# Kernel tuning notes

Measured on AMD Instinct MI355X. Metric: run time of the kernel, lower is better.

## Reference

```python
import jax, jax.numpy as jnp
import numpy as np

B, T, E, H, S = 4, 4096, 1024, 16, 64
D = E // H  # head_dim = 64


def setup_inputs() -> dict:
    key = jax.random.key(0)
    ks = jax.random.split(key, 8)
    sc = 0.02
    return {
        "x": jax.random.normal(ks[0], (B, T, E), jnp.float32),
        "state": jax.random.normal(ks[1], (H, B, S), jnp.float32),
        # stacked per-head params (torch Linear weight layout [out, in])
        "A_w": jax.random.normal(ks[2], (H, S, S), jnp.float32) * sc,
        "A_b": jnp.zeros((H, S), jnp.float32),
        "C_w": jax.random.normal(ks[3], (H, D, S), jnp.float32) * sc,
        "C_b": jnp.zeros((H, D), jnp.float32),
        "sm": jax.random.uniform(ks[4], (H, S, D), jnp.float32),  # torch.rand init
        "Wo": jax.random.normal(ks[5], (E, E), jnp.float32) * sc,
        "bo": jnp.zeros((E,), jnp.float32),
    }


def reference(x, state, A_w, A_b, C_w, C_b, sm, Wo, bo):
    b, t, e = x.shape
    h, s = A_b.shape
    d = e // h
    xh = x.reshape(b, t, h, d)  # [B,T,H,D]
    # A(state): state[i].detach() @ A_w[i].T + A_b[i]  -> [H,B,S]
    a_state = jnp.einsum('hbj,hij->hbi', jax.lax.stop_gradient(state), A_w) + A_b[:, None, :]
    # semiseparable_matrix @ x_head^T, transposed back: [B,T,H,S]
    proj = jnp.einsum('hsd,bthd->bths', sm, xh)
    # broadcast A(state) over the sequence dim (faithful to the original)
    new_state = proj + a_state.transpose(1, 0, 2)[:, None]  # [B,T,H,S]
    # C(new_state): [B,T,H,D]
    out_h = jnp.einsum('bths,hds->bthd', new_state, C_w) + C_b
    # concat heads + output projection
    out = out_h.reshape(b, t, e) @ Wo.T + bo  # [B,T,E]
    new_state_stacked = new_state.transpose(2, 0, 1, 3)  # [H,B,T,S]
    return out, new_state_stacked
```

## Files before the change

kernel.cpp:

```cpp
#include <hip/hip_runtime.h>

#define Bz 4
#define Tz 4096
#define Ez 1024
#define Hz 16
#define Sz 64
#define Dz 64
#define MTz (Bz*Tz)

using f32x4  = __attribute__((ext_vector_type(4))) float;
using short8 = __attribute__((ext_vector_type(8))) short;

__device__ __forceinline__ unsigned f2bf(float f){
  unsigned u = __builtin_bit_cast(unsigned, f);
  u = u + 0x7FFFu + ((u >> 16) & 1u);
  return (u >> 16);
}

#define GLL16(gp, lp) __builtin_amdgcn_global_load_lds( \
    (const __attribute__((address_space(1))) unsigned int*)(gp), \
    (__attribute__((address_space(3))) unsigned int*)(lp), 16, 0, 0)

__global__ __launch_bounds__(256) void k1_pre(const float* __restrict__ state,
                                              const float* __restrict__ A_w,
                                              const float* __restrict__ A_b,
                                              const float* __restrict__ C_w,
                                              const float* __restrict__ sm,
                                              float* __restrict__ a_state,
                                              float* __restrict__ Mh,
                                              unsigned short* __restrict__ smB){
  const int blk = blockIdx.x, tid = threadIdx.x;
  const int h = blk >> 2, q4 = blk & 3;
  {
    const int d = q4*16 + (tid >> 4), dp0 = (tid & 15)*4;
    const float* cw  = C_w + (size_t)(h*64 + d)*64;
    const float* smh = sm + (size_t)h*4096 + dp0;
    float ax=0.f, ay=0.f, az=0.f, aw=0.f;
    #pragma unroll 8
    for (int s = 0; s < 64; ++s){
      float c = cw[s];
      float4 m4 = *(const float4*)&smh[s*64];
      ax += c*m4.x; ay += c*m4.y; az += c*m4.z; aw += c*m4.w;
    }
    *(float4*)&Mh[(size_t)h*4096 + d*64 + dp0] = make_float4(ax,ay,az,aw);
  }
  {
    int gi = blk*1024 + tid*4;
    float4 v = *(const float4*)&sm[gi];
    uint2 pk = make_uint2(f2bf(v.x) | (f2bf(v.y)<<16), f2bf(v.z) | (f2bf(v.w)<<16));
    *(uint2*)&smB[gi] = pk;
  }
  if (q4 == 0){
    const int b = tid >> 6, s = tid & 63;
    const float* aw = A_w + (size_t)(h*64 + s)*64;
    const float* st = state + (size_t)(h*4 + b)*64;
    float a0=A_b[h*64+s], a1=0.f, a2=0.f, a3=0.f;
    #pragma unroll 4
    for (int j = 0; j < 64; j += 4){
      a0 += aw[j]*st[j]; a1 += aw[j+1]*st[j+1];
      a2 += aw[j+2]*st[j+2]; a3 += aw[j+3]*st[j+3];
    }
    a_state[(h*4 + b)*64 + s] = (a0+a1)+(a2+a3);
  }
}

__global__ __launch_bounds__(256) void k2_pre(const float* __restrict__ Wo,
                                              const float* __restrict__ Mh,
                                              const float* __restrict__ C_w,
                                              const float* __restrict__ C_b,
                                              const float* __restrict__ a_state,
                                              unsigned short* __restrict__ Wb,
                                              float* __restrict__ bias_f){
  const int blk = blockIdx.x, tid = threadIdx.x;
  if (blk < 1024){
    const int e = blk, h = tid >> 4, dp0 = (tid & 15)*4;
    const float* wo = Wo + (size_t)e*1024 + h*64;
    const float* mh = Mh + (size_t)h*4096 + dp0;
    float ax=0.f, ay=0.f, az=0.f, aw=0.f;
    #pragma unroll 8
    for (int d = 0; d < 64; ++d){
      float c = wo[d];
      float4 m4 = *(const float4*)&mh[d*64];
      ax += c*m4.x; ay += c*m4.y; az += c*m4.z; aw += c*m4.w;
    }
    uint2 pk = make_uint2(f2bf(ax) | (f2bf(ay)<<16), f2bf(az) | (f2bf(aw)<<16));
    *(uint2*)&Wb[(size_t)e*1024 + h*64 + dp0] = pk;
  } else {
    int o = (blk - 1024)*256 + tid;
    int b = o >> 10, f = o & 1023;
    int h = f >> 6, d = f & 63;
    const float* cw = C_w + (size_t)(h*64 + d)*64;
    const float* as = a_state + (size_t)(h*4 + b)*64;
    float a0=C_b[h*64+d], a1=0.f, a2=0.f, a3=0.f;
    #pragma unroll 4
    for (int s = 0; s < 64; s += 4){
      a0 += cw[s]*as[s]; a1 += cw[s+1]*as[s+1];
      a2 += cw[s+2]*as[s+2]; a3 += cw[s+3]*as[s+3];
    }
    bias_f[o] = (a0+a1)+(a2+a3);
  }
}

__global__ __launch_bounds__(64) void k3_const(const float* __restrict__ Wo,
                                               const float* __restrict__ bo,
                                               const float* __restrict__ bias_f,
                                               float* __restrict__ constb){
  const int blk = blockIdx.x, tid = threadIdx.x;
  const int b = blk >> 4, e = (blk & 15)*64 + tid;
  const float4* wo = (const float4*)(Wo + (size_t)e*1024);
  const float4* bf = (const float4*)(bias_f + (size_t)b*1024);
  float ax=0.f, ay=0.f, az=0.f, aw=0.f;
  for (int f4 = 0; f4 < 256; ++f4){
    float4 w = wo[f4], v = bf[f4];
    ax += w.x*v.x; ay += w.y*v.y; az += w.z*v.z; aw += w.w*v.w;
  }
  constb[b*1024 + e] = bo[e] + ((ax+ay)+(az+aw));
}

__global__ __launch_bounds__(256) void k4_ns(const float* __restrict__ x,
                                             const unsigned short* __restrict__ smB,
                                             const float* __restrict__ a_state,
                                             unsigned short* __restrict__ xb,
                                             float* __restrict__ out2){
  __shared__ alignas(16) unsigned short Xs[128*72];
  __shared__ alignas(16) unsigned short Ss[64*72];
  const int lin = blockIdx.x;
  const int tb = lin & 31, h = (lin >> 5) & 15, b = lin >> 9;
  const int tid = threadIdx.x;
  const int lane = tid & 63, w = tid >> 6;
  const int l15 = lane & 15, l4 = lane >> 4;

  {
    const unsigned short* src = smB + (size_t)h*4096;
    #pragma unroll
    for (int cc = 0; cc < 2; ++cc){
      int c = tid*2 + cc;
      int s = c >> 3, seg = c & 7;
      *(uint4*)&Ss[s*72 + seg*8] = *(const uint4*)&src[s*64 + seg*8];
    }
  }
  {
    const int row0 = b*Tz + tb*128;
    #pragma unroll
    for (int it = 0; it < 4; ++it){
      int id = it*256 + tid;
      int r = id >> 3, c8 = id & 7;
      const float* px = x + (size_t)(row0 + r)*1024 + h*64 + c8*8;
      float4 v0 = *(const float4*)px, v1 = *(const float4*)(px + 4);
      uint4 pk;
      pk.x = f2bf(v0.x) | (f2bf(v0.y)<<16);
      pk.y = f2bf(v0.z) | (f2bf(v0.w)<<16);
      pk.z = f2bf(v1.x) | (f2bf(v1.y)<<16);
      pk.w = f2bf(v1.z) | (f2bf(v1.w)<<16);
      *(uint4*)&Xs[r*72 + c8*8] = pk;
      *(uint4*)(xb + (size_t)(row0 + r)*1024 + h*64 + c8*8) = pk;
    }
  }
  __syncthreads();

  f32x4 acc[2][4];
  #pragma unroll
  for (int j = 0; j < 4; ++j){
    float4 as4 = *(const float4*)&a_state[(h*4 + b)*64 + j*16 + l4*4];
    f32x4 a0; a0[0]=as4.x; a0[1]=as4.y; a0[2]=as4.z; a0[3]=as4.w;
    acc[0][j] = a0; acc[1][j] = a0;
  }
  #pragma unroll
  for (int kk = 0; kk < 2; ++kk){
    short8 a[2], bb[4];
    #pragma unroll
    for (int i = 0; i < 2; ++i)
      a[i] = *(const short8*)(&Xs[(w*32 + i*16 + l15)*72 + kk*32 + l4*8]);
    #pragma unroll
    for (int j = 0; j < 4; ++j)
      bb[j] = *(const short8*)(&Ss[(j*16 + l15)*72 + kk*32 + l4*8]);
    #pragma unroll
    for (int i = 0; i < 2; ++i)
      #pragma unroll
      for (int j = 0; j < 4; ++j)
        acc[i][j] = __builtin_amdgcn_mfma_f32_16x16x32_bf16(bb[j], a[i], acc[i][j], 0, 0, 0);
  }
  const size_t base = (size_t)h*1048576 + ((size_t)b*4096 + tb*128)*64;
  #pragma unroll
  for (int i = 0; i < 2; ++i)
    #pragma unroll
    for (int j = 0; j < 4; ++j){
      float4 o = make_float4(acc[i][j][0], acc[i][j][1], acc[i][j][2], acc[i][j][3]);
      *(float4*)(out2 + base + (size_t)(w*32 + i*16 + l15)*64 + j*16 + l4*4) = o;
    }
}

__global__ __launch_bounds__(512, 2) void k5_gemm(const unsigned short* __restrict__ xb,
                                                  const unsigned short* __restrict__ Wb,
                                                  const float* __restrict__ constb,
                                                  float* __restrict__ out){
  __shared__ alignas(16) unsigned short lds[4][2][8192];
  const int blk = blockIdx.x;
  const int swz = (blk & 7)*32 + (blk >> 3);
  const int bm = (swz >> 2)*256, bn = (swz & 3)*256;
  const int tid = threadIdx.x;
  const int lane = tid & 63, w = tid >> 6;
  const int l15 = lane & 15, l4 = lane >> 4;
  const int wr = w >> 2, wc = w & 3;

  const unsigned short* srcA[2];
  const unsigned short* srcB[2];
  #pragma unroll
  for (int q = 0; q < 2; ++q){
    int L = q*512 + w*64 + lane;
    int b = ((L>>2)&1) ^ ((L>>4)&1);
    int r = (L>>3)*2 + b;
    int g = (L&3) ^ ((((L>>3)&1)<<1) | b);
    srcA[q] = xb + (size_t)(bm + r)*1024 + g*8;
    srcB[q] = Wb + (size_t)(bn + r)*1024 + g*8;
  }
  const int dstoff = w*64*8;
  const int lane_off = ((l15*4 + l4) ^ (l15 & 7))*8;

  #pragma unroll
  for (int t = 0; t < 3; ++t){
    #pragma unroll
    for (int q = 0; q < 2; ++q) GLL16(srcA[q] + t*32, &lds[t][0][q*4096 + dstoff]);
    #pragma unroll
    for (int q = 0; q < 2; ++q) GLL16(srcB[q] + t*32, &lds[t][1][q*4096 + dstoff]);
  }
  asm volatile("s_waitcnt vmcnt(8)" ::: "memory");
  __builtin_amdgcn_s_barrier();
  asm volatile("" ::: "memory");

  f32x4 acc[8][4] = {};

  for (int t = 0; t < 32; ++t){
    const unsigned short* At = &lds[t & 3][0][0];
    const unsigned short* Bt = &lds[t & 3][1][0];
    const int ts = (t + 3) & 3;
    short8 bfr[4], afr[4];
    #pragma unroll
    for (int j = 0; j < 4; ++j)
      bfr[j] = *(const short8*)(Bt + (wc*64 + j*16)*32 + lane_off);
    #pragma unroll
    for (int i = 0; i < 4; ++i)
      afr[i] = *(const short8*)(At + (wr*128 + i*16)*32 + lane_off);
    if (t < 29){
      #pragma unroll
      for (int q = 0; q < 2; ++q) GLL16(srcA[q] + (t+3)*32, &lds[ts][0][q*4096 + dstoff]);
    }
    __builtin_amdgcn_s_setprio(1);
    #pragma unroll
    for (int i = 0; i < 4; ++i)
      #pragma unroll
      for (int j = 0; j < 4; ++j)
        acc[i][j] = __builtin_amdgcn_mfma_f32_16x16x32_bf16(bfr[j], afr[i], acc[i][j], 0, 0, 0);
    __builtin_amdgcn_s_setprio(0);
    #pragma unroll
    for (int i = 0; i < 4; ++i)
      afr[i] = *(const short8*)(At + (wr*128 + (4 + i)*16)*32 + lane_off);
    if (t < 29){
      #pragma unroll
      for (int q = 0; q < 2; ++q) GLL16(srcB[q] + (t+3)*32, &lds[ts][1][q*4096 + dstoff]);
    }
    __builtin_amdgcn_s_setprio(1);
    #pragma unroll
    for (int i = 0; i < 4; ++i)
      #pragma unroll
      for (int j = 0; j < 4; ++j)
        acc[4+i][j] = __builtin_amdgcn_mfma_f32_16x16x32_bf16(bfr[j], afr[i], acc[4+i][j], 0, 0, 0);
    __builtin_amdgcn_s_setprio(0);
    if (t < 29)       asm volatile("s_waitcnt vmcnt(8)" ::: "memory");
    else if (t == 29) asm volatile("s_waitcnt vmcnt(4)" ::: "memory");
    else if (t == 30) asm volatile("s_waitcnt vmcnt(0)" ::: "memory");
    if (t < 31){
      __builtin_amdgcn_s_barrier();
      asm volatile("" ::: "memory");
    }
  }

  const int bb = bm >> 12;
  #pragma unroll
  for (int j = 0; j < 4; ++j){
    int n0 = bn + wc*64 + j*16 + l4*4;
    float4 cv = *(const float4*)&constb[bb*1024 + n0];
    #pragma unroll
    for (int i = 0; i < 8; ++i){
      int trow = bm + wr*128 + i*16 + l15;
      float4 o = make_float4(acc[i][j][0] + cv.x, acc[i][j][1] + cv.y,
                             acc[i][j][2] + cv.z, acc[i][j][3] + cv.w);
      *(float4*)(out + (size_t)trow*1024 + n0) = o;
    }
  }
}

extern "C" void kernel_launch(void* const* d_in, const int* in_sizes, int n_in,
                              void* d_out, int out_size, void* d_ws, size_t ws_size,
                              hipStream_t stream){
  const float* x     = (const float*)d_in[0];
  const float* state = (const float*)d_in[1];
  const float* A_w   = (const float*)d_in[2];
  const float* A_b   = (const float*)d_in[3];
  const float* C_w   = (const float*)d_in[4];
  const float* C_b   = (const float*)d_in[5];
  const float* sm    = (const float*)d_in[6];
  const float* Wo    = (const float*)d_in[7];
  const float* bo    = (const float*)d_in[8];
  float* out  = (float*)d_out;
  float* out2 = out + (size_t)MTz*Ez;

  char* ws = (char*)d_ws;
  float* a_state          = (float*)(ws + 0);
  float* Mh               = (float*)(ws + 16384);
  float* bias_f           = (float*)(ws + 278528);
  float* constb           = (float*)(ws + 294912);
  unsigned short* smB     = (unsigned short*)(ws + 311296);
  unsigned short* Wb      = (unsigned short*)(ws + 442368);
  unsigned short* xb      = (unsigned short*)(ws + 2539520);

  k1_pre<<<64, 256, 0, stream>>>(state, A_w, A_b, C_w, sm, a_state, Mh, smB);
  k2_pre<<<1040, 256, 0, stream>>>(Wo, Mh, C_w, C_b, a_state, Wb, bias_f);
  k3_const<<<64, 64, 0, stream>>>(Wo, bo, bias_f, constb);
  k4_ns<<<2048, 256, 0, stream>>>(x, smB, a_state, xb, out2);
  k5_gemm<<<256, 512, 0, stream>>>(xb, Wb, constb, out);
}
```

Baseline: 119.1 us.

## Fragment-major A layout loaded directly to registers; merge precompute kernels

k4_ns now writes the bf16 activations in an MFMA-fragment-major layout. The GEMM reads its A operand straight from global memory into double-buffered registers, so only B is staged through LDS, which cuts LDS traffic and footprint. The five launches become four: the precompute kernels are merged into two, and the sm-to-bf16 conversion moves into k4_ns. The risk is exposed global-load latency on A, and the merged precompute kernels now run on far fewer blocks (16 and 80), which may serialize them.

```diff
diff --git a/kernel.cpp b/kernel.cpp
--- a/kernel.cpp
+++ b/kernel.cpp
@@ -21,18 +21,34 @@
     (const __attribute__((address_space(1))) unsigned int*)(gp), \
     (__attribute__((address_space(3))) unsigned int*)(lp), 16, 0, 0)
 
-__global__ __launch_bounds__(256) void k1_pre(const float* __restrict__ state,
+__global__ __launch_bounds__(256) void p0_pre(const float* __restrict__ state,
                                               const float* __restrict__ A_w,
                                               const float* __restrict__ A_b,
                                               const float* __restrict__ C_w,
+                                              const float* __restrict__ C_b,
                                               const float* __restrict__ sm,
                                               float* __restrict__ a_state,
                                               float* __restrict__ Mh,
-                                              unsigned short* __restrict__ smB){
-  const int blk = blockIdx.x, tid = threadIdx.x;
-  const int h = blk >> 2, q4 = blk & 3;
+                                              float* __restrict__ bias_f){
+  __shared__ float asl[4][64];
+  const int h = blockIdx.x, tid = threadIdx.x;
   {
-    const int d = q4*16 + (tid >> 4), dp0 = (tid & 15)*4;
+    const int b = tid >> 6, s = tid & 63;
+    const float* aw = A_w + (size_t)(h*64 + s)*64;
+    const float* st = state + (size_t)(h*4 + b)*64;
+    float a0=A_b[h*64+s], a1=0.f, a2=0.f, a3=0.f;
+    #pragma unroll 4
+    for (int j = 0; j < 64; j += 4){
+      a0 += aw[j]*st[j]; a1 += aw[j+1]*st[j+1];
+      a2 += aw[j+2]*st[j+2]; a3 += aw[j+3]*st[j+3];
+    }
+    float v = (a0+a1)+(a2+a3);
+    a_state[(h*4 + b)*64 + s] = v;
+    asl[b][s] = v;
+  }
+  #pragma unroll
+  for (int q = 0; q < 4; ++q){
+    const int d = q*16 + (tid >> 4), dp0 = (tid & 15)*4;
     const float* cw  = C_w + (size_t)(h*64 + d)*64;
     const float* smh = sm + (size_t)h*4096 + dp0;
     float ax=0.f, ay=0.f, az=0.f, aw=0.f;
@@ -44,83 +60,67 @@
     }
     *(float4*)&Mh[(size_t)h*4096 + d*64 + dp0] = make_float4(ax,ay,az,aw);
   }
+  __syncthreads();
   {
-    int gi = blk*1024 + tid*4;
-    float4 v = *(const float4*)&sm[gi];
-    uint2 pk = make_uint2(f2bf(v.x) | (f2bf(v.y)<<16), f2bf(v.z) | (f2bf(v.w)<<16));
-    *(uint2*)&smB[gi] = pk;
-  }
-  if (q4 == 0){
-    const int b = tid >> 6, s = tid & 63;
-    const float* aw = A_w + (size_t)(h*64 + s)*64;
-    const float* st = state + (size_t)(h*4 + b)*64;
-    float a0=A_b[h*64+s], a1=0.f, a2=0.f, a3=0.f;
-    #pragma unroll 4
-    for (int j = 0; j < 64; j += 4){
-      a0 += aw[j]*st[j]; a1 += aw[j+1]*st[j+1];
-      a2 += aw[j+2]*st[j+2]; a3 += aw[j+3]*st[j+3];
-    }
-    a_state[(h*4 + b)*64 + s] = (a0+a1)+(a2+a3);
-  }
-}
-
-__global__ __launch_bounds__(256) void k2_pre(const float* __restrict__ Wo,
-                                              const float* __restrict__ Mh,
-                                              const float* __restrict__ C_w,
-                                              const float* __restrict__ C_b,
-                                              const float* __restrict__ a_state,
-                                              unsigned short* __restrict__ Wb,
-                                              float* __restrict__ bias_f){
-  const int blk = blockIdx.x, tid = threadIdx.x;
-  if (blk < 1024){
-    const int e = blk, h = tid >> 4, dp0 = (tid & 15)*4;
-    const float* wo = Wo + (size_t)e*1024 + h*64;
-    const float* mh = Mh + (size_t)h*4096 + dp0;
-    float ax=0.f, ay=0.f, az=0.f, aw=0.f;
-    #pragma unroll 8
-    for (int d = 0; d < 64; ++d){
-      float c = wo[d];
-      float4 m4 = *(const float4*)&mh[d*64];
-      ax += c*m4.x; ay += c*m4.y; az += c*m4.z; aw += c*m4.w;
-    }
-    uint2 pk = make_uint2(f2bf(ax) | (f2bf(ay)<<16), f2bf(az) | (f2bf(aw)<<16));
-    *(uint2*)&Wb[(size_t)e*1024 + h*64 + dp0] = pk;
-  } else {
-    int o = (blk - 1024)*256 + tid;
-    int b = o >> 10, f = o & 1023;
-    int h = f >> 6, d = f & 63;
+    const int b = tid >> 6, d = tid & 63;
     const float* cw = C_w + (size_t)(h*64 + d)*64;
-    const float* as = a_state + (size_t)(h*4 + b)*64;
     float a0=C_b[h*64+d], a1=0.f, a2=0.f, a3=0.f;
     #pragma unroll 4
     for (int s = 0; s < 64; s += 4){
-      a0 += cw[s]*as[s]; a1 += cw[s+1]*as[s+1];
-      a2 += cw[s+2]*as[s+2]; a3 += cw[s+3]*as[s+3];
-    }
-    bias_f[o] = (a0+a1)+(a2+a3);
-  }
-}
-
-__global__ __launch_bounds__(64) void k3_const(const float* __restrict__ Wo,
-                                               const float* __restrict__ bo,
-                                               const float* __restrict__ bias_f,
-                                               float* __restrict__ constb){
+      a0 += cw[s]*asl[b][s]; a1 += cw[s+1]*asl[b][s+1];
+      a2 += cw[s+2]*asl[b][s+2]; a3 += cw[s+3]*asl[b][s+3];
+    }
+    bias_f[b*1024 + h*64 + d] = (a0+a1)+(a2+a3);
+  }
+}
+
+__global__ __launch_bounds__(256) void p1_pre(const float* __restrict__ Wo,
+                                              const float* __restrict__ Mh,
+                                              const float* __restrict__ bias_f,
+                                              const float* __restrict__ bo,
+                                              unsigned short* __restrict__ Wb,
+                                              float* __restrict__ constb){
   const int blk = blockIdx.x, tid = threadIdx.x;
-  const int b = blk >> 4, e = (blk & 15)*64 + tid;
-  const float4* wo = (const float4*)(Wo + (size_t)e*1024);
-  const float4* bf = (const float4*)(bias_f + (size_t)b*1024);
-  float ax=0.f, ay=0.f, az=0.f, aw=0.f;
-  for (int f4 = 0; f4 < 256; ++f4){
-    float4 w = wo[f4], v = bf[f4];
-    ax += w.x*v.x; ay += w.y*v.y; az += w.z*v.z; aw += w.w*v.w;
-  }
-  constb[b*1024 + e] = bo[e] + ((ax+ay)+(az+aw));
+  if (blk < 64){
+    const int e = blk*16 + (tid >> 4), dp0 = (tid & 15)*4;
+    #pragma unroll 4
+    for (int h = 0; h < 16; ++h){
+      const float* wo = Wo + (size_t)e*1024 + h*64;
+      const float* mh = Mh + (size_t)h*4096 + dp0;
+      float ax=0.f, ay=0.f, az=0.f, aw=0.f;
+      #pragma unroll 4
+      for (int d4 = 0; d4 < 16; ++d4){
+        float4 w4 = *(const float4*)&wo[d4*4];
+        float4 m0 = *(const float4*)&mh[(d4*4+0)*64];
+        float4 m1 = *(const float4*)&mh[(d4*4+1)*64];
+        float4 m2 = *(const float4*)&mh[(d4*4+2)*64];
+        float4 m3 = *(const float4*)&mh[(d4*4+3)*64];
+        ax += w4.x*m0.x + w4.y*m1.x + w4.z*m2.x + w4.w*m3.x;
+        ay += w4.x*m0.y + w4.y*m1.y + w4.z*m2.y + w4.w*m3.y;
+        az += w4.x*m0.z + w4.y*m1.z + w4.z*m2.z + w4.w*m3.z;
+        aw += w4.x*m0.w + w4.y*m1.w + w4.z*m2.w + w4.w*m3.w;
+      }
+      uint2 pk = make_uint2(f2bf(ax) | (f2bf(ay)<<16), f2bf(az) | (f2bf(aw)<<16));
+      *(uint2*)&Wb[(size_t)e*1024 + h*64 + dp0] = pk;
+    }
+  } else {
+    int idx = (blk - 64)*256 + tid;
+    int b = idx >> 10, e = idx & 1023;
+    const float4* wo = (const float4*)(Wo + (size_t)e*1024);
+    const float4* bf = (const float4*)(bias_f + (size_t)b*1024);
+    float ax=0.f, ay=0.f, az=0.f, aw=0.f;
+    for (int f4 = 0; f4 < 256; ++f4){
+      float4 w = wo[f4], v = bf[f4];
+      ax += w.x*v.x; ay += w.y*v.y; az += w.z*v.z; aw += w.w*v.w;
+    }
+    constb[b*1024 + e] = bo[e] + ((ax+ay)+(az+aw));
+  }
 }
 
 __global__ __launch_bounds__(256) void k4_ns(const float* __restrict__ x,
-                                             const unsigned short* __restrict__ smB,
+                                             const float* __restrict__ sm,
                                              const float* __restrict__ a_state,
-                                             unsigned short* __restrict__ xb,
+                                             unsigned short* __restrict__ xb2,
                                              float* __restrict__ out2){
   __shared__ alignas(16) unsigned short Xs[128*72];
   __shared__ alignas(16) unsigned short Ss[64*72];
@@ -131,12 +131,14 @@
   const int l15 = lane & 15, l4 = lane >> 4;
 
   {
-    const unsigned short* src = smB + (size_t)h*4096;
-    #pragma unroll
-    for (int cc = 0; cc < 2; ++cc){
-      int c = tid*2 + cc;
-      int s = c >> 3, seg = c & 7;
-      *(uint4*)&Ss[s*72 + seg*8] = *(const uint4*)&src[s*64 + seg*8];
+    const float* src = sm + (size_t)h*4096;
+    #pragma unroll
+    for (int cc = 0; cc < 4; ++cc){
+      int c = cc*256 + tid;
+      int s = c >> 4, c4 = c & 15;
+      float4 v = *(const float4*)&src[s*64 + c4*4];
+      uint2 pk = make_uint2(f2bf(v.x) | (f2bf(v.y)<<16), f2bf(v.z) | (f2bf(v.w)<<16));
+      *(uint2*)&Ss[s*72 + c4*4] = pk;
     }
   }
   {
@@ -153,7 +155,10 @@
       pk.z = f2bf(v1.x) | (f2bf(v1.y)<<16);
       pk.w = f2bf(v1.z) | (f2bf(v1.w)<<16);
       *(uint4*)&Xs[r*72 + c8*8] = pk;
-      *(uint4*)(xb + (size_t)(row0 + r)*1024 + h*64 + c8*8) = pk;
+      int rg = row0 + r;
+      int kt = 2*h + (c8 >> 2), l4c = c8 & 3;
+      size_t dst = ((size_t)((rg >> 4)*32 + kt)*16 + (rg & 15))*32 + l4c*8;
+      *(uint4*)(xb2 + dst) = pk;
     }
   }
   __syncthreads();
@@ -190,11 +195,11 @@
     }
 }
 
-__global__ __launch_bounds__(512, 2) void k5_gemm(const unsigned short* __restrict__ xb,
+__global__ __launch_bounds__(512, 2) void k5_gemm(const unsigned short* __restrict__ xb2,
                                                   const unsigned short* __restrict__ Wb,
                                                   const float* __restrict__ constb,
                                                   float* __restrict__ out){
-  __shared__ alignas(16) unsigned short lds[4][2][8192];
+  __shared__ alignas(16) unsigned short ldsB[4][8192];
   const int blk = blockIdx.x;
   const int swz = (blk & 7)*32 + (blk >> 3);
   const int bm = (swz >> 2)*256, bn = (swz & 3)*256;
@@ -203,77 +208,113 @@
   const int l15 = lane & 15, l4 = lane >> 4;
   const int wr = w >> 2, wc = w & 3;
 
-  const unsigned short* srcA[2];
   const unsigned short* srcB[2];
   #pragma unroll
   for (int q = 0; q < 2; ++q){
     int L = q*512 + w*64 + lane;
-    int b = ((L>>2)&1) ^ ((L>>4)&1);
-    int r = (L>>3)*2 + b;
-    int g = (L&3) ^ ((((L>>3)&1)<<1) | b);
-    srcA[q] = xb + (size_t)(bm + r)*1024 + g*8;
+    int bbt = ((L>>2)&1) ^ ((L>>4)&1);
+    int r = (L>>3)*2 + bbt;
+    int g = (L&3) ^ ((((L>>3)&1)<<1) | bbt);
     srcB[q] = Wb + (size_t)(bn + r)*1024 + g*8;
   }
   const int dstoff = w*64*8;
   const int lane_off = ((l15*4 + l4) ^ (l15 & 7))*8;
 
+  const unsigned short* aP = xb2 + ((size_t)((bm >> 4) + wr*8)*32)*512 + l15*32 + l4*8;
+
+  f32x4 acc[8][4] = {};
+  short8 Aa[8], Ab[8];
+
   #pragma unroll
   for (int t = 0; t < 3; ++t){
     #pragma unroll
-    for (int q = 0; q < 2; ++q) GLL16(srcA[q] + t*32, &lds[t][0][q*4096 + dstoff]);
-    #pragma unroll
-    for (int q = 0; q < 2; ++q) GLL16(srcB[q] + t*32, &lds[t][1][q*4096 + dstoff]);
-  }
-  asm volatile("s_waitcnt vmcnt(8)" ::: "memory");
+    for (int q = 0; q < 2; ++q) GLL16(srcB[q] + t*32, &ldsB[t][q*4096 + dstoff]);
+  }
+  #pragma unroll
+  for (int i = 0; i < 8; ++i) Aa[i] = *(const short8*)(aP + i*16384);
+  asm volatile("s_waitcnt vmcnt(0)" ::: "memory");
   __builtin_amdgcn_s_barrier();
   asm volatile("" ::: "memory");
 
-  f32x4 acc[8][4] = {};
-
-  for (int t = 0; t < 32; ++t){
-    const unsigned short* At = &lds[t & 3][0][0];
-    const unsigned short* Bt = &lds[t & 3][1][0];
-    const int ts = (t + 3) & 3;
-    short8 bfr[4], afr[4];
-    #pragma unroll
-    for (int j = 0; j < 4; ++j)
-      bfr[j] = *(const short8*)(Bt + (wc*64 + j*16)*32 + lane_off);
-    #pragma unroll
-    for (int i = 0; i < 4; ++i)
-      afr[i] = *(const short8*)(At + (wr*128 + i*16)*32 + lane_off);
-    if (t < 29){
-      #pragma unroll
-      for (int q = 0; q < 2; ++q) GLL16(srcA[q] + (t+3)*32, &lds[ts][0][q*4096 + dstoff]);
-    }
-    __builtin_amdgcn_s_setprio(1);
-    #pragma unroll
-    for (int i = 0; i < 4; ++i)
-      #pragma unroll
-      for (int j = 0; j < 4; ++j)
-        acc[i][j] = __builtin_amdgcn_mfma_f32_16x16x32_bf16(bfr[j], afr[i], acc[i][j], 0, 0, 0);
-    __builtin_amdgcn_s_setprio(0);
-    #pragma unroll
-    for (int i = 0; i < 4; ++i)
-      afr[i] = *(const short8*)(At + (wr*128 + (4 + i)*16)*32 + lane_off);
-    if (t < 29){
-      #pragma unroll
-      for (int q = 0; q < 2; ++q) GLL16(srcB[q] + (t+3)*32, &lds[ts][1][q*4096 + dstoff]);
-    }
-    __builtin_amdgcn_s_setprio(1);
-    #pragma unroll
-    for (int i = 0; i < 4; ++i)
-      #pragma unroll
-      for (int j = 0; j < 4; ++j)
-        acc[4+i][j] = __builtin_amdgcn_mfma_f32_16x16x32_bf16(bfr[j], afr[i], acc[4+i][j], 0, 0, 0);
-    __builtin_amdgcn_s_setprio(0);
-    if (t < 29)       asm volatile("s_waitcnt vmcnt(8)" ::: "memory");
-    else if (t == 29) asm volatile("s_waitcnt vmcnt(4)" ::: "memory");
-    else if (t == 30) asm volatile("s_waitcnt vmcnt(0)" ::: "memory");
-    if (t < 31){
-      __builtin_amdgcn_s_barrier();
-      asm volatile("" ::: "memory");
-    }
-  }
+#define K5_TILE(T, CUR, NXT)                                                        \
+  {                                                                                 \
+    const int t_ = (T);                                                             \
+    const unsigned short* Bt = &ldsB[t_ & 3][0];                                    \
+    short8 bfr0 = *(const short8*)(Bt + (wc*64 +  0)*32 + lane_off);                \
+    short8 bfr1 = *(const short8*)(Bt + (wc*64 + 16)*32 + lane_off);                \
+    short8 bfr2 = *(const short8*)(Bt + (wc*64 + 32)*32 + lane_off);                \
+    short8 bfr3 = *(const short8*)(Bt + (wc*64 + 48)*32 + lane_off);                \
+    if (t_ < 31){                                                                   \
+      NXT[0] = *(const short8*)(aP + 0*16384 + (t_+1)*512);                         \
+      NXT[1] = *(const short8*)(aP + 1*16384 + (t_+1)*512);                         \
+      NXT[2] = *(const short8*)(aP + 2*16384 + (t_+1)*512);                         \
+      NXT[3] = *(const short8*)(aP + 3*16384 + (t_+1)*512);                         \
+    }                                                                               \
+    __builtin_amdgcn_s_setprio(1);                                                  \
+    acc[0][0]=__builtin_amdgcn_mfma_f32_16x16x32_bf16(bfr0,CUR[0],acc[0][0],0,0,0); \
+    acc[0][1]=__builtin_amdgcn_mfma_f32_16x16x32_bf16(bfr1,CUR[0],acc[0][1],0,0,0); \
+    acc[0][2]=__builtin_amdgcn_mfma_f32_16x16x32_bf16(bfr2,CUR[0],acc[0][2],0,0,0); \
+    acc[0][3]=__builtin_amdgcn_mfma_f32_16x16x32_bf16(bfr3,CUR[0],acc[0][3],0,0,0); \
+    acc[1][0]=__builtin_amdgcn_mfma_f32_16x16x32_bf16(bfr0,CUR[1],acc[1][0],0,0,0); \
+    acc[1][1]=__builtin_amdgcn_mfma_f32_16x16x32_bf16(bfr1,CUR[1],acc[1][1],0,0,0); \
+    acc[1][2]=__builtin_amdgcn_mfma_f32_16x16x32_bf16(bfr2,CUR[1],acc[1][2],0,0,0); \
+    acc[1][3]=__builtin_amdgcn_mfma_f32_16x16x32_bf16(bfr3,CUR[1],acc[1][3],0,0,0); \
+    __builtin_amdgcn_s_setprio(0);                                                  \
+    if (t_ < 31){                                                                   \
+      NXT[4] = *(const short8*)(aP + 4*16384 + (t_+1)*512);                         \
+      NXT[5] = *(const short8*)(aP + 5*16384 + (t_+1)*512);                         \
+      NXT[6] = *(const short8*)(aP + 6*16384 + (t_+1)*512);                         \
+      NXT[7] = *(const short8*)(aP + 7*16384 + (t_+1)*512);                         \
+    }                                                                               \
+    __builtin_amdgcn_s_setprio(1);                                                  \
+    acc[2][0]=__builtin_amdgcn_mfma_f32_16x16x32_bf16(bfr0,CUR[2],acc[2][0],0,0,0); \
+    acc[2][1]=__builtin_amdgcn_mfma_f32_16x16x32_bf16(bfr1,CUR[2],acc[2][1],0,0,0); \
+    acc[2][2]=__builtin_amdgcn_mfma_f32_16x16x32_bf16(bfr2,CUR[2],acc[2][2],0,0,0); \
+    acc[2][3]=__builtin_amdgcn_mfma_f32_16x16x32_bf16(bfr3,CUR[2],acc[2][3],0,0,0); \
+    acc[3][0]=__builtin_amdgcn_mfma_f32_16x16x32_bf16(bfr0,CUR[3],acc[3][0],0,0,0); \
+    acc[3][1]=__builtin_amdgcn_mfma_f32_16x16x32_bf16(bfr1,CUR[3],acc[3][1],0,0,0); \
+    acc[3][2]=__builtin_amdgcn_mfma_f32_16x16x32_bf16(bfr2,CUR[3],acc[3][2],0,0,0); \
+    acc[3][3]=__builtin_amdgcn_mfma_f32_16x16x32_bf16(bfr3,CUR[3],acc[3][3],0,0,0); \
+    __builtin_amdgcn_s_setprio(0);                                                  \
+    if (t_ <= 28){                                                                  \
+      GLL16(srcB[0] + (t_+3)*32, &ldsB[(t_+3) & 3][0*4096 + dstoff]);               \
+    }                                                                               \
+    __builtin_amdgcn_s_setprio(1);                                                  \
+    acc[4][0]=__builtin_amdgcn_mfma_f32_16x16x32_bf16(bfr0,CUR[4],acc[4][0],0,0,0); \
+    acc[4][1]=__builtin_amdgcn_mfma_f32_16x16x32_bf16(bfr1,CUR[4],acc[4][1],0,0,0); \
+    acc[4][2]=__builtin_amdgcn_mfma_f32_16x16x32_bf16(bfr2,CUR[4],acc[4][2],0,0,0); \
+    acc[4][3]=__builtin_amdgcn_mfma_f32_16x16x32_bf16(bfr3,CUR[4],acc[4][3],0,0,0); \
+    acc[5][0]=__builtin_amdgcn_mfma_f32_16x16x32_bf16(bfr0,CUR[5],acc[5][0],0,0,0); \
+    acc[5][1]=__builtin_amdgcn_mfma_f32_16x16x32_bf16(bfr1,CUR[5],acc[5][1],0,0,0); \
+    acc[5][2]=__builtin_amdgcn_mfma_f32_16x16x32_bf16(bfr2,CUR[5],acc[5][2],0,0,0); \
+    acc[5][3]=__builtin_amdgcn_mfma_f32_16x16x32_bf16(bfr3,CUR[5],acc[5][3],0,0,0); \
+    __builtin_amdgcn_s_setprio(0);                                                  \
+    if (t_ <= 28){                                                                  \
+      GLL16(srcB[1] + (t_+3)*32, &ldsB[(t_+3) & 3][1*4096 + dstoff]);               \
+    }                                                                               \
+    __builtin_amdgcn_s_setprio(1);                                                  \
+    acc[6][0]=__builtin_amdgcn_mfma_f32_16x16x32_bf16(bfr0,CUR[6],acc[6][0],0,0,0); \
+    acc[6][1]=__builtin_amdgcn_mfma_f32_16x16x32_bf16(bfr1,CUR[6],acc[6][1],0,0,0); \
+    acc[6][2]=__builtin_amdgcn_mfma_f32_16x16x32_bf16(bfr2,CUR[6],acc[6][2],0,0,0); \
+    acc[6][3]=__builtin_amdgcn_mfma_f32_16x16x32_bf16(bfr3,CUR[6],acc[6][3],0,0,0); \
+    acc[7][0]=__builtin_amdgcn_mfma_f32_16x16x32_bf16(bfr0,CUR[7],acc[7][0],0,0,0); \
+    acc[7][1]=__builtin_amdgcn_mfma_f32_16x16x32_bf16(bfr1,CUR[7],acc[7][1],0,0,0); \
+    acc[7][2]=__builtin_amdgcn_mfma_f32_16x16x32_bf16(bfr2,CUR[7],acc[7][2],0,0,0); \
+    acc[7][3]=__builtin_amdgcn_mfma_f32_16x16x32_bf16(bfr3,CUR[7],acc[7][3],0,0,0); \
+    __builtin_amdgcn_s_setprio(0);                                                  \
+    if (t_ <= 28)      { asm volatile("s_waitcnt vmcnt(2)" ::: "memory"); }         \
+    else if (t_ < 31)  { asm volatile("s_waitcnt vmcnt(0)" ::: "memory"); }         \
+    if (t_ < 31){                                                                   \
+      __builtin_amdgcn_s_barrier();                                                 \
+      asm volatile("" ::: "memory");                                                \
+    }                                                                               \
+  }
+
+  for (int tt = 0; tt < 16; ++tt){
+    K5_TILE(2*tt,     Aa, Ab);
+    K5_TILE(2*tt + 1, Ab, Aa);
+  }
+#undef K5_TILE
 
   const int bb = bm >> 12;
   #pragma unroll
@@ -310,13 +351,11 @@
   float* Mh               = (float*)(ws + 16384);
   float* bias_f           = (float*)(ws + 278528);
   float* constb           = (float*)(ws + 294912);
-  unsigned short* smB     = (unsigned short*)(ws + 311296);
-  unsigned short* Wb      = (unsigned short*)(ws + 442368);
-  unsigned short* xb      = (unsigned short*)(ws + 2539520);
-
-  k1_pre<<<64, 256, 0, stream>>>(state, A_w, A_b, C_w, sm, a_state, Mh, smB);
-  k2_pre<<<1040, 256, 0, stream>>>(Wo, Mh, C_w, C_b, a_state, Wb, bias_f);
-  k3_const<<<64, 64, 0, stream>>>(Wo, bo, bias_f, constb);
-  k4_ns<<<2048, 256, 0, stream>>>(x, smB, a_state, xb, out2);
-  k5_gemm<<<256, 512, 0, stream>>>(xb, Wb, constb, out);
-}
+  unsigned short* Wb      = (unsigned short*)(ws + 311296);
+  unsigned short* xb2     = (unsigned short*)(ws + 2408448);
+
+  p0_pre<<<16, 256, 0, stream>>>(state, A_w, A_b, C_w, C_b, sm, a_state, Mh, bias_f);
+  p1_pre<<<80, 256, 0, stream>>>(Wo, Mh, bias_f, bo, Wb, constb);
+  k4_ns<<<2048, 256, 0, stream>>>(x, sm, a_state, xb2, out2);
+  k5_gemm<<<256, 512, 0, stream>>>(xb2, Wb, constb, out);
+}
```

Result: slower. 151.9 us (+27.5%).

## Merge preprocessing kernels into two launches and convert sm to bf16 inline

Applied to the files above, without the earlier changes.

Collapses the three small preprocessing kernels into two. p0 computes a_state, Mh and bias_f per head, passing a_state through shared memory. p1 computes the folded bf16 weight Wb and constb in the same launch. The separate bf16 copy of sm is removed and k4 converts sm from fp32 as it loads it into LDS. This removes one launch and one intermediate buffer, but each preprocessing kernel now runs far fewer blocks (16 and 80) doing more serial work per thread, which could leave the preprocessing stage latency-bound.

```diff
diff --git a/kernel.cpp b/kernel.cpp
--- a/kernel.cpp
+++ b/kernel.cpp
@@ -21,18 +21,34 @@
     (const __attribute__((address_space(1))) unsigned int*)(gp), \
     (__attribute__((address_space(3))) unsigned int*)(lp), 16, 0, 0)
 
-__global__ __launch_bounds__(256) void k1_pre(const float* __restrict__ state,
+__global__ __launch_bounds__(256) void p0_pre(const float* __restrict__ state,
                                               const float* __restrict__ A_w,
                                               const float* __restrict__ A_b,
                                               const float* __restrict__ C_w,
+                                              const float* __restrict__ C_b,
                                               const float* __restrict__ sm,
                                               float* __restrict__ a_state,
                                               float* __restrict__ Mh,
-                                              unsigned short* __restrict__ smB){
-  const int blk = blockIdx.x, tid = threadIdx.x;
-  const int h = blk >> 2, q4 = blk & 3;
+                                              float* __restrict__ bias_f){
+  __shared__ float asl[4][64];
+  const int h = blockIdx.x, tid = threadIdx.x;
   {
-    const int d = q4*16 + (tid >> 4), dp0 = (tid & 15)*4;
+    const int b = tid >> 6, s = tid & 63;
+    const float* aw = A_w + (size_t)(h*64 + s)*64;
+    const float* st = state + (size_t)(h*4 + b)*64;
+    float a0=A_b[h*64+s], a1=0.f, a2=0.f, a3=0.f;
+    #pragma unroll 4
+    for (int j = 0; j < 64; j += 4){
+      a0 += aw[j]*st[j]; a1 += aw[j+1]*st[j+1];
+      a2 += aw[j+2]*st[j+2]; a3 += aw[j+3]*st[j+3];
+    }
+    float v = (a0+a1)+(a2+a3);
+    a_state[(h*4 + b)*64 + s] = v;
+    asl[b][s] = v;
+  }
+  #pragma unroll
+  for (int q = 0; q < 4; ++q){
+    const int d = q*16 + (tid >> 4), dp0 = (tid & 15)*4;
     const float* cw  = C_w + (size_t)(h*64 + d)*64;
     const float* smh = sm + (size_t)h*4096 + dp0;
     float ax=0.f, ay=0.f, az=0.f, aw=0.f;
@@ -44,81 +60,65 @@
     }
     *(float4*)&Mh[(size_t)h*4096 + d*64 + dp0] = make_float4(ax,ay,az,aw);
   }
+  __syncthreads();
   {
-    int gi = blk*1024 + tid*4;
-    float4 v = *(const float4*)&sm[gi];
-    uint2 pk = make_uint2(f2bf(v.x) | (f2bf(v.y)<<16), f2bf(v.z) | (f2bf(v.w)<<16));
-    *(uint2*)&smB[gi] = pk;
-  }
-  if (q4 == 0){
-    const int b = tid >> 6, s = tid & 63;
-    const float* aw = A_w + (size_t)(h*64 + s)*64;
-    const float* st = state + (size_t)(h*4 + b)*64;
-    float a0=A_b[h*64+s], a1=0.f, a2=0.f, a3=0.f;
-    #pragma unroll 4
-    for (int j = 0; j < 64; j += 4){
-      a0 += aw[j]*st[j]; a1 += aw[j+1]*st[j+1];
-      a2 += aw[j+2]*st[j+2]; a3 += aw[j+3]*st[j+3];
-    }
-    a_state[(h*4 + b)*64 + s] = (a0+a1)+(a2+a3);
-  }
-}
-
-__global__ __launch_bounds__(256) void k2_pre(const float* __restrict__ Wo,
-                                              const float* __restrict__ Mh,
-                                              const float* __restrict__ C_w,
-                                              const float* __restrict__ C_b,
-                                              const float* __restrict__ a_state,
-                                              unsigned short* __restrict__ Wb,
-                                              float* __restrict__ bias_f){
-  const int blk = blockIdx.x, tid = threadIdx.x;
-  if (blk < 1024){
-    const int e = blk, h = tid >> 4, dp0 = (tid & 15)*4;
-    const float* wo = Wo + (size_t)e*1024 + h*64;
-    const float* mh = Mh + (size_t)h*4096 + dp0;
-    float ax=0.f, ay=0.f, az=0.f, aw=0.f;
-    #pragma unroll 8
-    for (int d = 0; d < 64; ++d){
-      float c = wo[d];
-      float4 m4 = *(const float4*)&mh[d*64];
-      ax += c*m4.x; ay += c*m4.y; az += c*m4.z; aw += c*m4.w;
-    }
-    uint2 pk = make_uint2(f2bf(ax) | (f2bf(ay)<<16), f2bf(az) | (f2bf(aw)<<16));
-    *(uint2*)&Wb[(size_t)e*1024 + h*64 + dp0] = pk;
-  } else {
-    int o = (blk - 1024)*256 + tid;
-    int b = o >> 10, f = o & 1023;
-    int h = f >> 6, d = f & 63;
+    const int b = tid >> 6, d = tid & 63;
     const float* cw = C_w + (size_t)(h*64 + d)*64;
-    const float* as = a_state + (size_t)(h*4 + b)*64;
     float a0=C_b[h*64+d], a1=0.f, a2=0.f, a3=0.f;
     #pragma unroll 4
     for (int s = 0; s < 64; s += 4){
-      a0 += cw[s]*as[s]; a1 += cw[s+1]*as[s+1];
-      a2 += cw[s+2]*as[s+2]; a3 += cw[s+3]*as[s+3];
-    }
-    bias_f[o] = (a0+a1)+(a2+a3);
-  }
-}
-
-__global__ __launch_bounds__(64) void k3_const(const float* __restrict__ Wo,
-                                               const float* __restrict__ bo,
-                                               const float* __restrict__ bias_f,
-                                               float* __restrict__ constb){
+      a0 += cw[s]*asl[b][s]; a1 += cw[s+1]*asl[b][s+1];
+      a2 += cw[s+2]*asl[b][s+2]; a3 += cw[s+3]*asl[b][s+3];
+    }
+    bias_f[b*1024 + h*64 + d] = (a0+a1)+(a2+a3);
+  }
+}
+
+__global__ __launch_bounds__(256) void p1_pre(const float* __restrict__ Wo,
+                                              const float* __restrict__ Mh,
+                                              const float* __restrict__ bias_f,
+                                              const float* __restrict__ bo,
+                                              unsigned short* __restrict__ Wb,
+                                              float* __restrict__ constb){
   const int blk = blockIdx.x, tid = threadIdx.x;
-  const int b = blk >> 4, e = (blk & 15)*64 + tid;
-  const float4* wo = (const float4*)(Wo + (size_t)e*1024);
-  const float4* bf = (const float4*)(bias_f + (size_t)b*1024);
-  float ax=0.f, ay=0.f, az=0.f, aw=0.f;
-  for (int f4 = 0; f4 < 256; ++f4){
-    float4 w = wo[f4], v = bf[f4];
-    ax += w.x*v.x; ay += w.y*v.y; az += w.z*v.z; aw += w.w*v.w;
-  }
-  constb[b*1024 + e] = bo[e] + ((ax+ay)+(az+aw));
+  if (blk < 64){
+    const int e = blk*16 + (tid >> 4), dp0 = (tid & 15)*4;
+    #pragma unroll 4
+    for (int h = 0; h < 16; ++h){
+      const float* wo = Wo + (size_t)e*1024 + h*64;
+      const float* mh = Mh + (size_t)h*4096 + dp0;
+      float ax=0.f, ay=0.f, az=0.f, aw=0.f;
+      #pragma unroll 4
+      for (int d4 = 0; d4 < 16; ++d4){
+        float4 w4 = *(const float4*)&wo[d4*4];
+        float4 m0 = *(const float4*)&mh[(d4*4+0)*64];
+        float4 m1 = *(const float4*)&mh[(d4*4+1)*64];
+        float4 m2 = *(const float4*)&mh[(d4*4+2)*64];
+        float4 m3 = *(const float4*)&mh[(d4*4+3)*64];
+        ax += w4.x*m0.x + w4.y*m1.x + w4.z*m2.x + w4.w*m3.x;
+        ay += w4.x*m0.y + w4.y*m1.y + w4.z*m2.y + w4.w*m3.y;
+        az += w4.x*m0.z + w4.y*m1.z + w4.z*m2.z + w4.w*m3.z;
+        aw += w4.x*m0.w + w4.y*m1.w + w4.z*m2.w + w4.w*m3.w;
+      }
+      uint2 pk = make_uint2(f2bf(ax) | (f2bf(ay)<<16), f2bf(az) | (f2bf(aw)<<16));
+      *(uint2*)&Wb[(size_t)e*1024 + h*64 + dp0] = pk;
+    }
+  } else {
+    int idx = (blk - 64)*256 + tid;
+    int b = idx >> 10, e = idx & 1023;
+    const float4* wo = (const float4*)(Wo + (size_t)e*1024);
+    const float4* bf = (const float4*)(bias_f + (size_t)b*1024);
+    float ax=0.f, ay=0.f, az=0.f, aw=0.f;
+    for (int f4 = 0; f4 < 256; ++f4){
+      float4 w = wo[f4], v = bf[f4];
+      ax += w.x*v.x; ay += w.y*v.y; az += w.z*v.z; aw += w.w*v.w;
+    }
+    constb[b*1024 + e] = bo[e] + ((ax+ay)+(az+aw));
+  }
 }
 
 __global__ __launch_bounds__(256) void k4_ns(const float* __restrict__ x,
-                                             const unsigned short* __restrict__ smB,
+                                             const float* __restrict__ sm,
                                              const float* __restrict__ a_state,
                                              unsigned short* __restrict__ xb,
                                              float* __restrict__ out2){
@@ -131,12 +131,14 @@
   const int l15 = lane & 15, l4 = lane >> 4;
 
   {
-    const unsigned short* src = smB + (size_t)h*4096;
-    #pragma unroll
-    for (int cc = 0; cc < 2; ++cc){
-      int c = tid*2 + cc;
-      int s = c >> 3, seg = c & 7;
-      *(uint4*)&Ss[s*72 + seg*8] = *(const uint4*)&src[s*64 + seg*8];
+    const float* src = sm + (size_t)h*4096;
+    #pragma unroll
+    for (int cc = 0; cc < 4; ++cc){
+      int c = cc*256 + tid;
+      int s = c >> 4, c4 = c & 15;
+      float4 v = *(const float4*)&src[s*64 + c4*4];
+      uint2 pk = make_uint2(f2bf(v.x) | (f2bf(v.y)<<16), f2bf(v.z) | (f2bf(v.w)<<16));
+      *(uint2*)&Ss[s*72 + c4*4] = pk;
     }
   }
   {
@@ -310,13 +312,11 @@
   float* Mh               = (float*)(ws + 16384);
   float* bias_f           = (float*)(ws + 278528);
   float* constb           = (float*)(ws + 294912);
-  unsigned short* smB     = (unsigned short*)(ws + 311296);
-  unsigned short* Wb      = (unsigned short*)(ws + 442368);
-  unsigned short* xb      = (unsigned short*)(ws + 2539520);
-
-  k1_pre<<<64, 256, 0, stream>>>(state, A_w, A_b, C_w, sm, a_state, Mh, smB);
-  k2_pre<<<1040, 256, 0, stream>>>(Wo, Mh, C_w, C_b, a_state, Wb, bias_f);
-  k3_const<<<64, 64, 0, stream>>>(Wo, bo, bias_f, constb);
-  k4_ns<<<2048, 256, 0, stream>>>(x, smB, a_state, xb, out2);
+  unsigned short* Wb      = (unsigned short*)(ws + 311296);
+  unsigned short* xb      = (unsigned short*)(ws + 2408448);
+
+  p0_pre<<<16, 256, 0, stream>>>(state, A_w, A_b, C_w, C_b, sm, a_state, Mh, bias_f);
+  p1_pre<<<80, 256, 0, stream>>>(Wo, Mh, bias_f, bo, Wb, constb);
+  k4_ns<<<2048, 256, 0, stream>>>(x, sm, a_state, xb, out2);
   k5_gemm<<<256, 512, 0, stream>>>(xb, Wb, constb, out);
 }
```

New measurement: 139.6 us. 17.2% more time.
